# Kernel optimization log

Measured on AMD Instinct MI355X. Metric: run time of the kernel, lower is better.

Reference implementation:

```python
import jax, jax.numpy as jnp
import numpy as np

NUM_TAGS = 128
VOCAB = 50257
SEQ_LEN = 8192
START_TAG = 0   # tag2id['<s>'] in the original
END_TAG = 1     # vocab['</s>'] in the original (code quirk; treated as end-tag id)
NEG_INF = -10000.0


def setup_inputs() -> dict:
    key = jax.random.key(0)
    k1, k2, k3 = jax.random.split(key, 3)
    x = jax.random.randint(k1, (SEQ_LEN,), 0, VOCAB)
    emit_score = jax.random.normal(k2, (VOCAB, NUM_TAGS), dtype=jnp.float32)
    transitions = jax.random.normal(k3, (NUM_TAGS, NUM_TAGS), dtype=jnp.float32)
    return {"x": x, "emit_score": emit_score, "transitions": transitions}


def reference(x, emit_score, transitions):
    # CRF forward algorithm (log partition function z).
    # Original: per-timestep, per-tag python loops of log_sum_exp over
    # _score = alphas[:, None] + emit[ch_id][None, :] + transitions.
    # All num_tags updates at step t read the *old* alphas (the in-place
    # writes only touch _score's source after it was built), so this is the
    # standard vectorized recurrence: a logsumexp reduction over the prev-tag axis.
    emits = emit_score[x[1:]]  # [S-1, T] gathered emission scores
    init_alphas = jnp.full((NUM_TAGS,), NEG_INF, dtype=emit_score.dtype).at[START_TAG].set(0.0)

    def step(alphas, emit_t):
        # score[prev, cur] = alphas[prev] + emit_t[cur] + transitions[prev, cur]
        score = alphas[:, None] + emit_t[None, :] + transitions  # [T, T]
        return jax.nn.logsumexp(score, axis=0), None

    alphas, _ = jax.lax.scan(step, init_alphas, emits)
    z = jax.nn.logsumexp(alphas + transitions[:, END_TAG])  # scalar
    return z
```

## Files before the change

kernel.cpp:

```cpp
#include <hip/hip_runtime.h>

#define NTG 128
#define NSTEPS 8191
#define GCH 512
#define LCH 16
#define MATF16 (NTG*NTG)

typedef _Float16 half8v  __attribute__((ext_vector_type(8)));
typedef _Float16 half4v  __attribute__((ext_vector_type(4)));
typedef float    float4v __attribute__((ext_vector_type(4)));

__device__ __forceinline__ int su(int row, int col){
  return (row*NTG + col) ^ ((row & 15) << 3);
}

__device__ __forceinline__ float wave_max(float v){
#pragma unroll
  for (int m = 32; m >= 1; m >>= 1) v = fmaxf(v, __shfl_xor(v, m));
  return v;
}
__device__ __forceinline__ float wave_sum(float v){
#pragma unroll
  for (int m = 32; m >= 1; m >>= 1) v += __shfl_xor(v, m);
  return v;
}

__global__ void k_prep(const float* __restrict__ T, _Float16* __restrict__ En,
                       _Float16* __restrict__ Et){
  const int idx = blockIdx.x*256 + threadIdx.x;
  const int i = idx >> 7, j = idx & 127;
  const float v = __expf(T[idx]);
  En[idx] = (_Float16)v;
  Et[j*NTG + i] = (_Float16)v;
}

__global__ __launch_bounds__(512, 4)
void k_chunks(const int* __restrict__ x, const float* __restrict__ emit,
              const _Float16* __restrict__ Et, const _Float16* __restrict__ En,
              _Float16* __restrict__ Pt, double* __restrict__ scale)
{
  __shared__ _Float16 X[MATF16];
  __shared__ float red_g[2][8];

  const int t = threadIdx.x;
  const int lane = t & 63, wv = t >> 6;
  const int l15 = lane & 15, g4 = lane >> 4;
  const int g = blockIdx.x;
  const int s0 = g*LCH;
  const int nst = min(LCH, NSTEPS - s0);
  const int jA = wv*16 + l15;

  half8v aE[4];
#pragma unroll
  for (int ks=0; ks<4; ++ks)
    aE[ks] = *(const half8v*)(Et + jA*NTG + ks*32 + g4*8);

  double cacc;
  {
    const int tok = x[1+s0];
    const float* er = emit + (size_t)tok*NTG;
    const float2 me2 = *(const float2*)(er + (t&63)*2);
    const float m0 = wave_max(fmaxf(me2.x, me2.y));
    const float sa = __expf(me2.x - m0) * 0.0078125f;
    const float sb = __expf(me2.y - m0) * 0.0078125f;
    const int j0 = (t&63)*2;
    const unsigned int* ens = (const unsigned int*)En;
#pragma unroll
    for (int it=0; it<16; ++it){
      const int idx = it*512 + t;
      union { unsigned int u; _Float16 h[2]; } pk;
      pk.u = ens[idx];
      pk.h[0] = (_Float16)((float)pk.h[0]*sa);
      pk.h[1] = (_Float16)((float)pk.h[1]*sb);
      *(unsigned int*)&X[su(idx>>6, j0)] = pk.u;
    }
    cacc = (double)m0 + 4.852030263919617;
  }
  __syncthreads();

  float pscale = 1.0f;
  float4v accv[8];
  for (int s=1; s<nst; ++s){
    const int tok = x[1+s0+s];
    const float* er = emit + (size_t)tok*NTG;
    const float2 me2 = *(const float2*)(er + (t&63)*2);
    const float m = wave_max(fmaxf(me2.x, me2.y));
    const _Float16 hA = (_Float16)(__expf(er[jA] - m) * pscale);
    half8v ap[4];
#pragma unroll
    for (int ks=0; ks<4; ++ks) ap[ks] = aE[ks] * hA;

#pragma unroll
    for (int it=0; it<8; ++it) accv[it] = (float4v){0.f,0.f,0.f,0.f};

#pragma unroll
    for (int it=0; it<8; ++it){
      const int c = it*16 + l15;
      half8v bf[4];
#pragma unroll
      for (int ks=0; ks<4; ++ks)
        bf[ks] = *(const half8v*)&X[su(c, ks*32 + g4*8)];
#pragma unroll
      for (int ks=0; ks<4; ++ks)
        accv[it] = __builtin_amdgcn_mfma_f32_16x16x32_f16(ap[ks], bf[ks], accv[it], 0,0,0);
    }

    float gm = 0.f;
#pragma unroll
    for (int it=0; it<8; ++it)
#pragma unroll
      for (int r=0;r<4;r++) gm = fmaxf(gm, accv[it][r]);
    __syncthreads();
#pragma unroll
    for (int it=0; it<8; ++it){
      half4v h;
#pragma unroll
      for (int r=0;r<4;r++) h[r] = (_Float16)accv[it][r];
      *(half4v*)&X[su(it*16 + l15, wv*16 + g4*4)] = h;
    }
    gm = wave_max(gm);
    if (lane==0) red_g[s&1][wv] = gm;
    __syncthreads();
    float gmax = red_g[s&1][0];
#pragma unroll
    for (int q=1;q<8;q++) gmax = fmaxf(gmax, red_g[s&1][q]);
    pscale = 1.0f/gmax;
    cacc += (double)m + (double)__logf(gmax);
  }

  const float inv = pscale;
  unsigned int* pt = (unsigned int*)(Pt + (size_t)g*MATF16);
  const int ii = (t&63)*2;
#pragma unroll
  for (int it=0; it<16; ++it){
    const int uidx = it*512 + t;
    const int jj = uidx >> 6;
    union { unsigned int u; _Float16 h[2]; } pk;
    pk.h[0] = (_Float16)((float)X[su(ii,   jj)]*inv);
    pk.h[1] = (_Float16)((float)X[su(ii+1, jj)]*inv);
    pt[uidx] = pk.u;
  }
  if (t==0) scale[g] = cacc;
}

__global__ __launch_bounds__(512, 2)
void k_comb8(const _Float16* __restrict__ Pt_in, const double* __restrict__ Sin,
             _Float16* __restrict__ Pt_out, double* __restrict__ Sout)
{
  __shared__ _Float16 X[MATF16];
  __shared__ float red_g[2][8];
  const int t = threadIdx.x;
  const int lane = t & 63, wv = t >> 6;
  const int l15 = lane & 15, g4 = lane >> 4;
  const int p = blockIdx.x;
  const int jA = wv*16 + l15;

  {
    const unsigned int* src = (const unsigned int*)(Pt_in + (size_t)p*8*MATF16);
    const int i0 = (t&63)*2;
#pragma unroll
    for (int it=0; it<16; ++it){
      const int pos = it*512 + t;
      union { unsigned int u; _Float16 h[2]; } pk;
      pk.u = src[pos];
      const int j = pos >> 6;
      X[su(i0,   j)] = pk.h[0];
      X[su(i0+1, j)] = pk.h[1];
    }
  }
  __syncthreads();

  float pscale = 1.0f;
  double slog = 0.0;
  float4v accv[8];
  for (int mi=1; mi<8; ++mi){
    const _Float16* Yt = Pt_in + (size_t)(p*8+mi)*MATF16;
    half8v aB[4];
#pragma unroll
    for (int ks=0; ks<4; ++ks)
      aB[ks] = *(const half8v*)(Yt + jA*NTG + ks*32 + g4*8);

#pragma unroll
    for (int it=0; it<8; ++it) accv[it] = (float4v){0.f,0.f,0.f,0.f};

#pragma unroll
    for (int it=0; it<8; ++it){
      const int c = it*16 + l15;
      half8v bf[4];
#pragma unroll
      for (int ks=0; ks<4; ++ks)
        bf[ks] = *(const half8v*)&X[su(c, ks*32 + g4*8)];
#pragma unroll
      for (int ks=0; ks<4; ++ks)
        accv[it] = __builtin_amdgcn_mfma_f32_16x16x32_f16(aB[ks], bf[ks], accv[it], 0,0,0);
    }

    float gm = 0.f;
#pragma unroll
    for (int it=0; it<8; ++it)
#pragma unroll
      for (int r=0;r<4;r++){
        const float v = accv[it][r]*pscale;
        accv[it][r] = v;
        gm = fmaxf(gm, v);
      }
    __syncthreads();
#pragma unroll
    for (int it=0; it<8; ++it){
      half4v h;
#pragma unroll
      for (int r=0;r<4;r++) h[r] = (_Float16)accv[it][r];
      *(half4v*)&X[su(it*16 + l15, wv*16 + g4*4)] = h;
    }
    gm = wave_max(gm);
    if (lane==0) red_g[mi&1][wv] = gm;
    __syncthreads();
    float gmax = red_g[mi&1][0];
#pragma unroll
    for (int q=1;q<8;q++) gmax = fmaxf(gmax, red_g[mi&1][q]);
    pscale = 1.0f/gmax;
    slog += (double)__logf(gmax);
  }

  const float inv = pscale;
  unsigned int* pt = (unsigned int*)(Pt_out + (size_t)p*MATF16);
  const int ii = (t&63)*2;
#pragma unroll
  for (int it=0; it<16; ++it){
    const int uidx = it*512 + t;
    const int jj = uidx >> 6;
    union { unsigned int u; _Float16 h[2]; } pk;
    pk.h[0] = (_Float16)((float)X[su(ii,   jj)]*inv);
    pk.h[1] = (_Float16)((float)X[su(ii+1, jj)]*inv);
    pt[uidx] = pk.u;
  }
  if (t==0){
    double ssum = slog;
#pragma unroll
    for (int q=0;q<8;q++) ssum += Sin[p*8+q];
    Sout[p] = ssum;
  }
}

__global__ void k_final(const _Float16* __restrict__ PtC, const double* __restrict__ scC,
                        const float* __restrict__ T, float* __restrict__ out)
{
  __shared__ float u[2][NTG];
  __shared__ float red[4], red2[4];
  const int t = threadIdx.x;
  const int lane = t & 63, wv = t >> 6;

  double acc = 0.0;
#pragma unroll
  for (int q=0;q<8;q++) acc += scC[q];

  if (t < NTG) u[0][t] = (t==0) ? 1.f : 0.f;
  __syncthreads();

  int cur = 0;
  const int r = t >> 1, off = (t&1)*64;
  for (int k=0;k<8;k++){
    const _Float16* Y = PtC + (size_t)k*MATF16 + (size_t)r*NTG + off;
    float dot = 0.f;
#pragma unroll
    for (int q=0;q<8;q++){
      const half8v h = *(const half8v*)(Y + q*8);
#pragma unroll
      for (int e=0;e<8;e++) dot += (float)h[e]*u[cur][off + q*8 + e];
    }
    dot += __shfl_xor(dot, 1);
    if ((t&1)==0) u[cur^1][r] = dot;
    __syncthreads();
    cur ^= 1;
  }

  const float val = (t < NTG) ? (__logf(u[cur][t]) + T[t*NTG + 1]) : -3.0e38f;
  float mx = wave_max(val);
  if (lane==0) red[wv] = mx;
  __syncthreads();
  mx = fmaxf(fmaxf(red[0],red[1]), fmaxf(red[2],red[3]));
  const float e = (t < NTG) ? __expf(val - mx) : 0.f;
  const float s = wave_sum(e);
  if (lane==0) red2[wv] = s;
  __syncthreads();
  if (t==0){
    const double z = (double)mx + log((double)(red2[0]+red2[1]+red2[2]+red2[3])) + acc;
    out[0] = (float)z;
  }
}

extern "C" void kernel_launch(void* const* d_in, const int* in_sizes, int n_in,
                              void* d_out, int out_size, void* d_ws, size_t ws_size,
                              hipStream_t stream)
{
  const int*   x    = (const int*)d_in[0];
  const float* emit = (const float*)d_in[1];
  const float* T    = (const float*)d_in[2];
  float* out = (float*)d_out;

  _Float16* En  = (_Float16*)d_ws;
  _Float16* Et  = En  + MATF16;
  _Float16* PtA = Et  + MATF16;
  _Float16* PtB = PtA + (size_t)512*MATF16;
  _Float16* PtC = PtB + (size_t)64*MATF16;
  double* scA = (double*)(PtC + (size_t)8*MATF16);
  double* scB = scA + 512;
  double* scC = scB + 64;

  k_prep<<<64, 256, 0, stream>>>(T, En, Et);
  k_chunks<<<GCH, 512, 0, stream>>>(x, emit, Et, En, PtA, scA);
  k_comb8<<<64, 512, 0, stream>>>(PtA, scA, PtB, scB);
  k_comb8<<< 8, 512, 0, stream>>>(PtB, scB, PtC, scC);
  k_final<<<1, 256, 0, stream>>>(PtC, scC, T, out);
}
```

Measured before the change: 182.5 us.

## Double-buffer chunk matrices, retile waves 2x4, fuse exp(T) prep into chunk kernel

Drops the separate k_prep launch: each chunk block now computes exp(transitions) itself, both the A fragments and the initial matrix. The shared state matrix is double-buffered so each step needs one barrier instead of two. Waves are retiled as a 4x2 grid so each A fragment is reused across several column tiles. Emission scaling moves from the A operand into the output epilogue, and wave 0 prefetches the next step's emission row. k_comb8 gets the same double buffering plus register prefetch of the next B matrix. In exchange, every block redundantly evaluates exp over strided, uncoalesced transition reads, and register pressure rises.

```diff
diff --git a/kernel.cpp b/kernel.cpp
--- a/kernel.cpp
+++ b/kernel.cpp
@@ -25,220 +25,267 @@
   return v;
 }
 
-__global__ void k_prep(const float* __restrict__ T, _Float16* __restrict__ En,
-                       _Float16* __restrict__ Et){
-  const int idx = blockIdx.x*256 + threadIdx.x;
-  const int i = idx >> 7, j = idx & 127;
-  const float v = __expf(T[idx]);
-  En[idx] = (_Float16)v;
-  Et[j*NTG + i] = (_Float16)v;
+__device__ __forceinline__ float red8(const float* rg){
+  const float4v r0 = *(const float4v*)rg;
+  const float4v r1 = *(const float4v*)(rg+4);
+  return fmaxf(fmaxf(fmaxf(r0[0],r0[1]),fmaxf(r0[2],r0[3])),
+               fmaxf(fmaxf(r1[0],r1[1]),fmaxf(r1[2],r1[3])));
 }
 
 __global__ __launch_bounds__(512, 4)
 void k_chunks(const int* __restrict__ x, const float* __restrict__ emit,
-              const _Float16* __restrict__ Et, const _Float16* __restrict__ En,
-              _Float16* __restrict__ Pt, double* __restrict__ scale)
+              const float* __restrict__ T, _Float16* __restrict__ Pt,
+              double* __restrict__ scale)
 {
-  __shared__ _Float16 X[MATF16];
+  __shared__ _Float16 X[2][MATF16];
+  __shared__ float ehl[2][NTG];
   __shared__ float red_g[2][8];
 
-  const int t = threadIdx.x;
-  const int lane = t & 63, wv = t >> 6;
+  const int t = threadIdx.x, lane = t & 63, wv = t >> 6;
   const int l15 = lane & 15, g4 = lane >> 4;
-  const int g = blockIdx.x;
-  const int s0 = g*LCH;
+  const int wr = wv >> 1, wc = wv & 1;
+  const int g = blockIdx.x, s0 = g*LCH;
   const int nst = min(LCH, NSTEPS - s0);
-  const int jA = wv*16 + l15;
-
-  half8v aE[4];
-#pragma unroll
-  for (int ks=0; ks<4; ++ks)
-    aE[ks] = *(const half8v*)(Et + jA*NTG + ks*32 + g4*8);
-
-  double cacc;
+
+  half8v aE[2][4];
+#pragma unroll
+  for (int rt=0; rt<2; ++rt){
+    const int j = wr*32 + rt*16 + l15;
+#pragma unroll
+    for (int ks=0; ks<4; ++ks){
+      half8v a;
+#pragma unroll
+      for (int jj=0; jj<8; ++jj)
+        a[jj] = (_Float16)__expf(T[(ks*32 + g4*8 + jj)*NTG + j]);
+      aE[rt][ks] = a;
+    }
+  }
+
+  int tokv = 0;
+  if (wv==0) tokv = x[1 + s0 + min(lane, nst-1)];
+
+  double cacc = 0.0;
   {
-    const int tok = x[1+s0];
-    const float* er = emit + (size_t)tok*NTG;
-    const float2 me2 = *(const float2*)(er + (t&63)*2);
-    const float m0 = wave_max(fmaxf(me2.x, me2.y));
-    const float sa = __expf(me2.x - m0) * 0.0078125f;
-    const float sb = __expf(me2.y - m0) * 0.0078125f;
-    const int j0 = (t&63)*2;
-    const unsigned int* ens = (const unsigned int*)En;
+    const int tok0 = x[1+s0];
+    const float2 e0 = *(const float2*)(emit + (size_t)tok0*NTG + lane*2);
+    const float m0 = wave_max(fmaxf(e0.x, e0.y));
+    const float sa = __expf(e0.x - m0)*0.0078125f;
+    const float sb = __expf(e0.y - m0)*0.0078125f;
+    const int j0 = lane*2;
 #pragma unroll
     for (int it=0; it<16; ++it){
       const int idx = it*512 + t;
-      union { unsigned int u; _Float16 h[2]; } pk;
-      pk.u = ens[idx];
-      pk.h[0] = (_Float16)((float)pk.h[0]*sa);
-      pk.h[1] = (_Float16)((float)pk.h[1]*sb);
-      *(unsigned int*)&X[su(idx>>6, j0)] = pk.u;
-    }
-    cacc = (double)m0 + 4.852030263919617;
-  }
-  __syncthreads();
-
-  float pscale = 1.0f;
-  float4v accv[8];
+      const int i = idx >> 6;
+      const float2 tv = *(const float2*)(T + (size_t)i*NTG + j0);
+      union { unsigned u; _Float16 h[2]; } pk;
+      pk.h[0] = (_Float16)(__expf(tv.x)*sa);
+      pk.h[1] = (_Float16)(__expf(tv.y)*sb);
+      *(unsigned*)&X[1][su(i, j0)] = pk.u;
+    }
+    if (t==0) cacc = (double)m0 + 4.852030263919617;
+    if (wv==0){
+      const int tok1 = __shfl(tokv, 1);
+      const float2 e1 = *(const float2*)(emit + (size_t)tok1*NTG + lane*2);
+      const float m1 = wave_max(fmaxf(e1.x, e1.y));
+      *(float2*)&ehl[1][lane*2] = make_float2(__expf(e1.x-m1), __expf(e1.y-m1));
+      if (t==0) cacc += (double)m1;
+    }
+    if (t<8) red_g[0][t] = 1.0f;
+  }
+
+  float4v accv[2][4];
   for (int s=1; s<nst; ++s){
-    const int tok = x[1+s0+s];
-    const float* er = emit + (size_t)tok*NTG;
-    const float2 me2 = *(const float2*)(er + (t&63)*2);
-    const float m = wave_max(fmaxf(me2.x, me2.y));
-    const _Float16 hA = (_Float16)(__expf(er[jA] - m) * pscale);
-    half8v ap[4];
-#pragma unroll
-    for (int ks=0; ks<4; ++ks) ap[ks] = aE[ks] * hA;
-
-#pragma unroll
-    for (int it=0; it<8; ++it) accv[it] = (float4v){0.f,0.f,0.f,0.f};
-
-#pragma unroll
-    for (int it=0; it<8; ++it){
-      const int c = it*16 + l15;
+    __syncthreads();
+    const float gmax = red8(&red_g[(s-1)&1][0]);
+    const float pscale = 1.0f/gmax;
+    if (t==0) cacc += (double)__logf(gmax);
+
+#pragma unroll
+    for (int rt=0;rt<2;++rt)
+#pragma unroll
+      for (int ct=0;ct<4;++ct) accv[rt][ct] = (float4v){0.f,0.f,0.f,0.f};
+
+    const _Float16* __restrict__ Xs = X[s&1];
+#pragma unroll
+    for (int ct=0; ct<4; ++ct){
+      const int c = wc*64 + ct*16 + l15;
       half8v bf[4];
 #pragma unroll
-      for (int ks=0; ks<4; ++ks)
-        bf[ks] = *(const half8v*)&X[su(c, ks*32 + g4*8)];
-#pragma unroll
-      for (int ks=0; ks<4; ++ks)
-        accv[it] = __builtin_amdgcn_mfma_f32_16x16x32_f16(ap[ks], bf[ks], accv[it], 0,0,0);
+      for (int ks=0;ks<4;++ks)
+        bf[ks] = *(const half8v*)&Xs[su(c, ks*32 + g4*8)];
+#pragma unroll
+      for (int rt=0;rt<2;++rt)
+#pragma unroll
+        for (int ks=0;ks<4;++ks)
+          accv[rt][ct] = __builtin_amdgcn_mfma_f32_16x16x32_f16(aE[rt][ks], bf[ks], accv[rt][ct], 0,0,0);
+    }
+
+    if (wv==0 && s+1<nst){
+      const int tokn = __shfl(tokv, s+1);
+      const float2 en = *(const float2*)(emit + (size_t)tokn*NTG + lane*2);
+      const float mn = wave_max(fmaxf(en.x,en.y));
+      *(float2*)&ehl[(s+1)&1][lane*2] = make_float2(__expf(en.x-mn), __expf(en.y-mn));
+      if (t==0) cacc += (double)mn;
     }
 
     float gm = 0.f;
-#pragma unroll
-    for (int it=0; it<8; ++it)
-#pragma unroll
-      for (int r=0;r<4;r++) gm = fmaxf(gm, accv[it][r]);
-    __syncthreads();
-#pragma unroll
-    for (int it=0; it<8; ++it){
-      half4v h;
-#pragma unroll
-      for (int r=0;r<4;r++) h[r] = (_Float16)accv[it][r];
-      *(half4v*)&X[su(it*16 + l15, wv*16 + g4*4)] = h;
+    _Float16* __restrict__ Xd = X[(s+1)&1];
+#pragma unroll
+    for (int rt=0;rt<2;++rt){
+      const float4v eh4 = *(const float4v*)&ehl[s&1][wr*32 + rt*16 + g4*4];
+#pragma unroll
+      for (int ct=0;ct<4;++ct){
+        half4v h;
+#pragma unroll
+        for (int r=0;r<4;r++){
+          const float v = accv[rt][ct][r]*eh4[r]*pscale;
+          gm = fmaxf(gm, v);
+          h[r] = (_Float16)v;
+        }
+        *(half4v*)&Xd[su(wc*64 + ct*16 + l15, wr*32 + rt*16 + g4*4)] = h;
+      }
     }
     gm = wave_max(gm);
     if (lane==0) red_g[s&1][wv] = gm;
-    __syncthreads();
-    float gmax = red_g[s&1][0];
-#pragma unroll
-    for (int q=1;q<8;q++) gmax = fmaxf(gmax, red_g[s&1][q]);
-    pscale = 1.0f/gmax;
-    cacc += (double)m + (double)__logf(gmax);
-  }
-
-  const float inv = pscale;
-  unsigned int* pt = (unsigned int*)(Pt + (size_t)g*MATF16);
-  const int ii = (t&63)*2;
-#pragma unroll
-  for (int it=0; it<16; ++it){
-    const int uidx = it*512 + t;
-    const int jj = uidx >> 6;
-    union { unsigned int u; _Float16 h[2]; } pk;
-    pk.h[0] = (_Float16)((float)X[su(ii,   jj)]*inv);
-    pk.h[1] = (_Float16)((float)X[su(ii+1, jj)]*inv);
-    pt[uidx] = pk.u;
-  }
-  if (t==0) scale[g] = cacc;
+  }
+
+  __syncthreads();
+  {
+    const float gmaxF = red8(&red_g[(nst-1)&1][0]);
+    const float inv = 1.0f/gmaxF;
+    const _Float16* __restrict__ Xf = X[nst&1];
+    unsigned* pt = (unsigned*)(Pt + (size_t)g*MATF16);
+#pragma unroll
+    for (int it=0; it<16; ++it){
+      const int uidx = it*512 + t;
+      const int jj = uidx >> 6, ii = (uidx & 63)*2;
+      union { unsigned u; _Float16 h[2]; } pk;
+      pk.h[0] = (_Float16)((float)Xf[su(ii,   jj)]*inv);
+      pk.h[1] = (_Float16)((float)Xf[su(ii+1, jj)]*inv);
+      pt[uidx] = pk.u;
+    }
+    if (t==0) scale[g] = cacc + (double)__logf(gmaxF);
+  }
 }
 
 __global__ __launch_bounds__(512, 2)
 void k_comb8(const _Float16* __restrict__ Pt_in, const double* __restrict__ Sin,
              _Float16* __restrict__ Pt_out, double* __restrict__ Sout)
 {
-  __shared__ _Float16 X[MATF16];
+  __shared__ _Float16 X[2][MATF16];
   __shared__ float red_g[2][8];
-  const int t = threadIdx.x;
-  const int lane = t & 63, wv = t >> 6;
+  const int t = threadIdx.x, lane = t & 63, wv = t >> 6;
   const int l15 = lane & 15, g4 = lane >> 4;
+  const int wr = wv >> 1, wc = wv & 1;
   const int p = blockIdx.x;
-  const int jA = wv*16 + l15;
+  const _Float16* __restrict__ base = Pt_in + (size_t)p*8*MATF16;
 
   {
-    const unsigned int* src = (const unsigned int*)(Pt_in + (size_t)p*8*MATF16);
-    const int i0 = (t&63)*2;
+    const unsigned* src = (const unsigned*)base;
 #pragma unroll
     for (int it=0; it<16; ++it){
       const int pos = it*512 + t;
-      union { unsigned int u; _Float16 h[2]; } pk;
+      union { unsigned u; _Float16 h[2]; } pk;
       pk.u = src[pos];
-      const int j = pos >> 6;
-      X[su(i0,   j)] = pk.h[0];
-      X[su(i0+1, j)] = pk.h[1];
-    }
-  }
-  __syncthreads();
-
-  float pscale = 1.0f;
+      const int jj = pos >> 6, ii = (pos & 63)*2;
+      X[1][su(ii,   jj)] = pk.h[0];
+      X[1][su(ii+1, jj)] = pk.h[1];
+    }
+    if (t<8) red_g[0][t] = 1.0f;
+  }
+
+  half8v aB[2][4];
+#pragma unroll
+  for (int rt=0;rt<2;++rt)
+#pragma unroll
+    for (int ks=0;ks<4;++ks)
+      aB[rt][ks] = *(const half8v*)(base + MATF16 + (size_t)(wr*32+rt*16+l15)*NTG + ks*32 + g4*8);
+
   double slog = 0.0;
-  float4v accv[8];
+  float4v accv[2][4];
+#pragma unroll
   for (int mi=1; mi<8; ++mi){
-    const _Float16* Yt = Pt_in + (size_t)(p*8+mi)*MATF16;
-    half8v aB[4];
-#pragma unroll
-    for (int ks=0; ks<4; ++ks)
-      aB[ks] = *(const half8v*)(Yt + jA*NTG + ks*32 + g4*8);
-
-#pragma unroll
-    for (int it=0; it<8; ++it) accv[it] = (float4v){0.f,0.f,0.f,0.f};
-
-#pragma unroll
-    for (int it=0; it<8; ++it){
-      const int c = it*16 + l15;
+    __syncthreads();
+    const float gmax = red8(&red_g[(mi-1)&1][0]);
+    const float pscale = 1.0f/gmax;
+    if (t==0) slog += (double)__logf(gmax);
+
+#pragma unroll
+    for (int rt=0;rt<2;++rt)
+#pragma unroll
+      for (int ct=0;ct<4;++ct) accv[rt][ct] = (float4v){0.f,0.f,0.f,0.f};
+
+    const _Float16* __restrict__ Xs = X[mi&1];
+#pragma unroll
+    for (int ct=0; ct<4; ++ct){
+      const int c = wc*64 + ct*16 + l15;
       half8v bf[4];
 #pragma unroll
-      for (int ks=0; ks<4; ++ks)
-        bf[ks] = *(const half8v*)&X[su(c, ks*32 + g4*8)];
-#pragma unroll
-      for (int ks=0; ks<4; ++ks)
-        accv[it] = __builtin_amdgcn_mfma_f32_16x16x32_f16(aB[ks], bf[ks], accv[it], 0,0,0);
+      for (int ks=0;ks<4;++ks)
+        bf[ks] = *(const half8v*)&Xs[su(c, ks*32 + g4*8)];
+#pragma unroll
+      for (int rt=0;rt<2;++rt)
+#pragma unroll
+        for (int ks=0;ks<4;++ks)
+          accv[rt][ct] = __builtin_amdgcn_mfma_f32_16x16x32_f16(aB[rt][ks], bf[ks], accv[rt][ct], 0,0,0);
+    }
+
+    half8v aBn[2][4];
+    if (mi<7){
+#pragma unroll
+      for (int rt=0;rt<2;++rt)
+#pragma unroll
+        for (int ks=0;ks<4;++ks)
+          aBn[rt][ks] = *(const half8v*)(base + (size_t)(mi+1)*MATF16 + (size_t)(wr*32+rt*16+l15)*NTG + ks*32 + g4*8);
     }
 
     float gm = 0.f;
-#pragma unroll
-    for (int it=0; it<8; ++it)
-#pragma unroll
-      for (int r=0;r<4;r++){
-        const float v = accv[it][r]*pscale;
-        accv[it][r] = v;
-        gm = fmaxf(gm, v);
+    _Float16* __restrict__ Xd = X[(mi+1)&1];
+#pragma unroll
+    for (int rt=0;rt<2;++rt)
+#pragma unroll
+      for (int ct=0;ct<4;++ct){
+        half4v h;
+#pragma unroll
+        for (int r=0;r<4;r++){
+          const float v = accv[rt][ct][r]*pscale;
+          gm = fmaxf(gm, v);
+          h[r] = (_Float16)v;
+        }
+        *(half4v*)&Xd[su(wc*64 + ct*16 + l15, wr*32 + rt*16 + g4*4)] = h;
       }
-    __syncthreads();
-#pragma unroll
-    for (int it=0; it<8; ++it){
-      half4v h;
-#pragma unroll
-      for (int r=0;r<4;r++) h[r] = (_Float16)accv[it][r];
-      *(half4v*)&X[su(it*16 + l15, wv*16 + g4*4)] = h;
-    }
     gm = wave_max(gm);
     if (lane==0) red_g[mi&1][wv] = gm;
-    __syncthreads();
-    float gmax = red_g[mi&1][0];
-#pragma unroll
-    for (int q=1;q<8;q++) gmax = fmaxf(gmax, red_g[mi&1][q]);
-    pscale = 1.0f/gmax;
-    slog += (double)__logf(gmax);
-  }
-
-  const float inv = pscale;
-  unsigned int* pt = (unsigned int*)(Pt_out + (size_t)p*MATF16);
-  const int ii = (t&63)*2;
-#pragma unroll
-  for (int it=0; it<16; ++it){
-    const int uidx = it*512 + t;
-    const int jj = uidx >> 6;
-    union { unsigned int u; _Float16 h[2]; } pk;
-    pk.h[0] = (_Float16)((float)X[su(ii,   jj)]*inv);
-    pk.h[1] = (_Float16)((float)X[su(ii+1, jj)]*inv);
-    pt[uidx] = pk.u;
-  }
-  if (t==0){
-    double ssum = slog;
-#pragma unroll
-    for (int q=0;q<8;q++) ssum += Sin[p*8+q];
-    Sout[p] = ssum;
+
+    if (mi<7){
+#pragma unroll
+      for (int rt=0;rt<2;++rt)
+#pragma unroll
+        for (int ks=0;ks<4;++ks) aB[rt][ks] = aBn[rt][ks];
+    }
+  }
+
+  __syncthreads();
+  {
+    const float gmaxF = red8(&red_g[1][0]);
+    const float inv = 1.0f/gmaxF;
+    const _Float16* __restrict__ Xf = X[0];
+    unsigned* pt = (unsigned*)(Pt_out + (size_t)p*MATF16);
+#pragma unroll
+    for (int it=0; it<16; ++it){
+      const int uidx = it*512 + t;
+      const int jj = uidx >> 6, ii = (uidx & 63)*2;
+      union { unsigned u; _Float16 h[2]; } pk;
+      pk.h[0] = (_Float16)((float)Xf[su(ii,   jj)]*inv);
+      pk.h[1] = (_Float16)((float)Xf[su(ii+1, jj)]*inv);
+      pt[uidx] = pk.u;
+    }
+    if (t==0){
+      double ssum = slog + (double)__logf(gmaxF);
+#pragma unroll
+      for (int q=0;q<8;q++) ssum += Sin[p*8+q];
+      Sout[p] = ssum;
+    }
   }
 }
 
@@ -278,13 +325,13 @@
   float mx = wave_max(val);
   if (lane==0) red[wv] = mx;
   __syncthreads();
-  mx = fmaxf(fmaxf(red[0],red[1]), fmaxf(red[2],red[3]));
+  mx = fmaxf(red[0], red[1]);
   const float e = (t < NTG) ? __expf(val - mx) : 0.f;
   const float s = wave_sum(e);
   if (lane==0) red2[wv] = s;
   __syncthreads();
   if (t==0){
-    const double z = (double)mx + log((double)(red2[0]+red2[1]+red2[2]+red2[3])) + acc;
+    const double z = (double)mx + log((double)(red2[0]+red2[1])) + acc;
     out[0] = (float)z;
   }
 }
@@ -298,17 +345,14 @@
   const float* T    = (const float*)d_in[2];
   float* out = (float*)d_out;
 
-  _Float16* En  = (_Float16*)d_ws;
-  _Float16* Et  = En  + MATF16;
-  _Float16* PtA = Et  + MATF16;
+  _Float16* PtA = (_Float16*)d_ws;
   _Float16* PtB = PtA + (size_t)512*MATF16;
   _Float16* PtC = PtB + (size_t)64*MATF16;
   double* scA = (double*)(PtC + (size_t)8*MATF16);
   double* scB = scA + 512;
   double* scC = scB + 64;
 
-  k_prep<<<64, 256, 0, stream>>>(T, En, Et);
-  k_chunks<<<GCH, 512, 0, stream>>>(x, emit, Et, En, PtA, scA);
+  k_chunks<<<GCH, 512, 0, stream>>>(x, emit, T, PtA, scA);
   k_comb8<<<64, 512, 0, stream>>>(PtA, scA, PtB, scB);
   k_comb8<<< 8, 512, 0, stream>>>(PtB, scB, PtC, scC);
   k_final<<<1, 256, 0, stream>>>(PtC, scC, T, out);
```

After: 171.9 us. 5.8% less time.
